# Optimization experiments

Hardware: AMD Instinct MI355X
Metric: run time of the kernel (lower is better)

## Reference

```python
import jax, jax.numpy as jnp
import numpy as np

B, S, D, H = 2, 4096, 512, 8
HD = D // H


def setup_inputs() -> dict:
    key = jax.random.key(0)
    ks = jax.random.split(key, 11)
    s = 1.0 / np.sqrt(D)
    return {
        "queries": jax.random.normal(ks[0], (B, S, D), jnp.float32),
        "keys": jax.random.normal(ks[1], (B, S, D), jnp.float32),
        "values": jax.random.normal(ks[2], (B, S, D), jnp.float32),
        "Wq": jax.random.normal(ks[3], (D, D), jnp.float32) * s,
        "bq": jnp.zeros((D,), jnp.float32),
        "Wk": jax.random.normal(ks[4], (D, D), jnp.float32) * s,
        "bk": jnp.zeros((D,), jnp.float32),
        "Wv": jax.random.normal(ks[5], (D, D), jnp.float32) * s,
        "bv": jnp.zeros((D,), jnp.float32),
        "Wo": jax.random.normal(ks[6], (D, D), jnp.float32) * s,
        "bo": jnp.zeros((D,), jnp.float32),
    }


def reference(queries, keys, values, Wq, bq, Wk, bk, Wv, bv, Wo, bo):
    b = queries.shape[0]
    # Linear projections (torch Linear: x @ W.T + b; here W stored as [in, out])
    q = (queries @ Wq + bq).reshape(b, -1, H, HD)   # [B, Sq, H, HD]
    k = (keys @ Wk + bk).reshape(b, -1, H, HD)       # [B, Sk, H, HD]
    v = (values @ Wv + bv).reshape(b, -1, H, HD)     # [B, Sk, H, HD]
    logits = jnp.einsum('bqhd,bkhd->bhqk', q, k) / jnp.sqrt(jnp.float32(HD))
    attn = jax.nn.softmax(logits, axis=-1)           # [B, H, Sq, Sk]  (dropout_rate=0 -> identity)
    ctx = jnp.einsum('bhqk,bkhd->bqhd', attn, v).reshape(b, -1, H * HD)
    return ctx @ Wo + bo
```

## Files before the change

### kernel.cpp

```cpp
#include <hip/hip_runtime.h>
#include <hip/hip_bf16.h>

constexpr int B_  = 2;
constexpr int S_  = 4096;
constexpr int D_  = 512;
constexpr int H_  = 8;
constexpr int HD_ = 64;
constexpr int M_  = B_ * S_;

typedef __attribute__((ext_vector_type(8))) short short8;
typedef __attribute__((ext_vector_type(4))) float floatx4;

static __device__ __forceinline__ unsigned short f2bf(float f) {
    union { float f; unsigned u; } v; v.f = f;
    unsigned r = v.u + 0x7fffu + ((v.u >> 16) & 1u);
    return (unsigned short)(r >> 16);
}

static __device__ __forceinline__ unsigned pk2bf(float a, float b) {
#if __has_builtin(__builtin_amdgcn_cvt_pk_bf16_f32)
    typedef __attribute__((ext_vector_type(2))) __bf16 bf16x2_t;
    union { bf16x2_t v; unsigned u; } u;
    u.v = __builtin_amdgcn_cvt_pk_bf16_f32(a, b);
    return u.u;
#else
    return (unsigned)f2bf(a) | ((unsigned)f2bf(b) << 16);
#endif
}

#if __has_builtin(__builtin_amdgcn_exp2f)
#define EXP2(x) __builtin_amdgcn_exp2f(x)
#else
#define EXP2(x) exp2f(x)
#endif

#define QSCALE 0.18033688011110204f

static __device__ __forceinline__ void gl_lds16(const void* g, void* l) {
    typedef __attribute__((address_space(1))) const unsigned GU;
    typedef __attribute__((address_space(3))) unsigned LU;
    __builtin_amdgcn_global_load_lds((GU*)g, (LU*)l, 16, 0, 0);
}

__global__ __launch_bounds__(256) void xcast_kernel(
    const float* __restrict__ Xq, const float* __restrict__ Xk, const float* __restrict__ Xv,
    unsigned short* __restrict__ Y) {
    const int z = blockIdx.z;
    const float* X = z == 0 ? Xq : (z == 1 ? Xk : Xv);
    unsigned short* Yz = Y + (size_t)z * M_ * D_;
    const int n8 = M_ * D_ / 8;
    int i = blockIdx.x * 256 + threadIdx.x;
    const int stride = gridDim.x * 256;
    for (; i < n8; i += stride) {
        float4 a = *(const float4*)&X[(size_t)i * 8];
        float4 b = *(const float4*)&X[(size_t)i * 8 + 4];
        union { short8 s; unsigned u[4]; } p;
        p.u[0] = pk2bf(a.x, a.y); p.u[1] = pk2bf(a.z, a.w);
        p.u[2] = pk2bf(b.x, b.y); p.u[3] = pk2bf(b.z, b.w);
        *(short8*)&Yz[(size_t)i * 8] = p.s;
    }
}

__global__ __launch_bounds__(256) void wtrans_kernel(
    const float* __restrict__ Wq, const float* __restrict__ Wk,
    const float* __restrict__ Wv, const float* __restrict__ Wo,
    unsigned short* __restrict__ Tq, unsigned short* __restrict__ Tk,
    unsigned short* __restrict__ Tv, unsigned short* __restrict__ To) {
    const int z = blockIdx.z;
    const float* W = z == 0 ? Wq : (z == 1 ? Wk : (z == 2 ? Wv : Wo));
    unsigned short* Wt = z == 0 ? Tq : (z == 1 ? Tk : (z == 2 ? Tv : To));
    __shared__ float T[64][65];
    const int t = threadIdx.x;
    const int k0 = blockIdx.x * 64, n0 = blockIdx.y * 64;
#pragma unroll
    for (int i = 0; i < 4; ++i) {
        const int flat = t + 256 * i;
        const int kr = flat >> 4, nc = (flat & 15) * 4;
        float4 v = *(const float4*)&W[(size_t)(k0 + kr) * 512 + n0 + nc];
        T[kr][nc] = v.x; T[kr][nc + 1] = v.y; T[kr][nc + 2] = v.z; T[kr][nc + 3] = v.w;
    }
    __syncthreads();
#pragma unroll
    for (int i = 0; i < 4; ++i) {
        const int flat = t + 256 * i;
        const int nr = flat >> 4, kc = (flat & 15) * 4;
        ushort4 o4;
        o4.x = f2bf(T[kc][nr]);     o4.y = f2bf(T[kc + 1][nr]);
        o4.z = f2bf(T[kc + 2][nr]); o4.w = f2bf(T[kc + 3][nr]);
        *(ushort4*)&Wt[(size_t)(n0 + nr) * 512 + k0 + kc] = o4;
    }
}

template <int MODE>
__global__ __launch_bounds__(256, 3) void gemm_kernel(
    const unsigned short* __restrict__ Ab,
    const unsigned short* __restrict__ Wt,
    const float* __restrict__ b0, const float* __restrict__ b1, const float* __restrict__ b2,
    unsigned short* __restrict__ o0, unsigned short* __restrict__ o1,
    unsigned short* __restrict__ o2, float* __restrict__ of) {
    __shared__ unsigned short As[128 * 64];
    __shared__ unsigned short Bs[128 * 64];

    const int tid  = threadIdx.x;
    const int w    = tid >> 6;
    const int lane = tid & 63;
    const int n0   = blockIdx.x * 128;
    const int m0   = blockIdx.y * 128;
    const int lm   = lane & 15;
    const int lq   = lane >> 4;
    const int wm   = (w >> 1) * 64;
    const int wn   = (w & 1) * 64;

    const int z = MODE == 0 ? (n0 >> 9) : 0;
    const unsigned short* A = MODE == 0 ? Ab + (size_t)z * M_ * D_ : Ab;

    const int srow = lane >> 3;
    const int sch  = lane & 7;
    const int ca   = (sch ^ (srow & 7)) * 8;

    floatx4 acc[4][4];
#pragma unroll
    for (int i = 0; i < 4; ++i)
#pragma unroll
        for (int j = 0; j < 4; ++j) acc[i][j] = (floatx4)0.0f;

    for (int kb = 0; kb < 8; ++kb) {
        const int k0 = kb * 64;
        __syncthreads();
#pragma unroll
        for (int it = 0; it < 4; ++it) {
            const int r8 = w * 32 + it * 8;
            gl_lds16(&A [(size_t)(m0 + r8 + srow) * 512 + k0 + ca], &As[r8 * 64]);
            gl_lds16(&Wt[(size_t)(n0 + r8 + srow) * 512 + k0 + ca], &Bs[r8 * 64]);
        }
        __syncthreads();

        short8 af[2][4], bf[2][4];
#pragma unroll
        for (int ks = 0; ks < 2; ++ks)
#pragma unroll
            for (int i = 0; i < 4; ++i) {
                const int cc = ((ks * 4 + lq) ^ (lm & 7)) * 8;
                af[ks][i] = *(const short8*)&As[(wm + i * 16 + lm) * 64 + cc];
                bf[ks][i] = *(const short8*)&Bs[(wn + i * 16 + lm) * 64 + cc];
            }
#pragma unroll
        for (int ks = 0; ks < 2; ++ks)
#pragma unroll
            for (int mi = 0; mi < 4; ++mi)
#pragma unroll
                for (int ni = 0; ni < 4; ++ni)
                    acc[mi][ni] = __builtin_amdgcn_mfma_f32_16x16x32_bf16(
                        af[ks][mi], bf[ks][ni], acc[mi][ni], 0, 0, 0);
    }

    const float* bias = MODE == 0 ? (z == 0 ? b0 : (z == 1 ? b1 : b2)) : b0;
    const float scale = (MODE == 0 && z == 0) ? QSCALE : 1.0f;
    const int nl0 = n0 & 511;

    float bias_n[4];
#pragma unroll
    for (int ni = 0; ni < 4; ++ni) bias_n[ni] = bias[nl0 + wn + ni * 16 + lm];

#pragma unroll
    for (int mi = 0; mi < 4; ++mi) {
#pragma unroll
        for (int ni = 0; ni < 4; ++ni) {
            if (MODE == 1) {
                const int gn = n0 + wn + ni * 16 + lm;
#pragma unroll
                for (int r = 0; r < 4; ++r) {
                    const int gm = m0 + wm + mi * 16 + lq * 4 + r;
                    of[(size_t)gm * 512 + gn] = acc[mi][ni][r] + bias_n[ni];
                }
            } else {
                const int gnl = nl0 + wn + ni * 16 + lm;
                const int h = gnl >> 6, hd = gnl & 63;
                if (z == 2) {
                    const int gm = m0 + wm + mi * 16 + lq * 4;
                    const int b = gm >> 12, s = gm & 4095;
                    union { ushort4 s4; uint2 u; } o4;
                    o4.u.x = pk2bf(acc[mi][ni][0] + bias_n[ni], acc[mi][ni][1] + bias_n[ni]);
                    o4.u.y = pk2bf(acc[mi][ni][2] + bias_n[ni], acc[mi][ni][3] + bias_n[ni]);
                    *(ushort4*)&o2[(((size_t)(b * 8 + h)) * 64 + hd) * 4096 + s] = o4.s4;
                } else {
                    unsigned short* out = z == 0 ? o0 : o1;
#pragma unroll
                    for (int r = 0; r < 4; ++r) {
                        const int gm = m0 + wm + mi * 16 + lq * 4 + r;
                        const int b = gm >> 12, s = gm & 4095;
                        const float vv = (acc[mi][ni][r] + bias_n[ni]) * scale;
                        out[(((size_t)(b * 8 + h)) * 4096 + s) * 64 + hd] = f2bf(vv);
                    }
                }
            }
        }
    }
}

__global__ __launch_bounds__(256, 2) void flash_kernel(
    const unsigned short* __restrict__ Q, const unsigned short* __restrict__ K,
    const unsigned short* __restrict__ Vt, unsigned short* __restrict__ ctx) {
    __shared__ unsigned short Ks[64 * 64];
    __shared__ unsigned short Vs[64 * 64];
    __shared__ unsigned short Ps[4][16 * 64];

    const int tid = threadIdx.x;
    const int w   = tid >> 6;
    const int l   = tid & 63;
    const int lm  = l & 15;
    const int lq  = l >> 4;
    const int q0  = blockIdx.x * 128;
    const int bh  = blockIdx.y;

    const size_t base = (size_t)bh * S_ * HD_;
    const unsigned short* Qg = Q + base;
    const unsigned short* Kg = K + base;
    const unsigned short* Vg = Vt + base;

    short8 qf[2][2];
#pragma unroll
    for (int qn = 0; qn < 2; ++qn) {
        const unsigned short* qp = &Qg[(size_t)(q0 + w * 32 + qn * 16 + lm) * 64];
        qf[qn][0] = *(const short8*)(qp + lq * 8);
        qf[qn][1] = *(const short8*)(qp + 32 + lq * 8);
    }

    short8 ones;
#pragma unroll
    for (int j = 0; j < 8; ++j) ones[j] = (short)0x3F80;

    floatx4 o[2][4];
#pragma unroll
    for (int qn = 0; qn < 2; ++qn)
#pragma unroll
        for (int i = 0; i < 4; ++i) o[qn][i] = (floatx4)0.0f;
    floatx4 ls[2];
    ls[0] = (floatx4)0.0f; ls[1] = (floatx4)0.0f;

    const int sr  = tid >> 3, sch = tid & 7;
    const int sw0 = sr * 64 + ((sch ^ (sr & 7)) * 8);
    const int sw1 = (sr + 32) * 64 + ((sch ^ (sr & 7)) * 8);
    const int lm7 = lm & 7;

    short8 kr0, kr1, vr0, vr1;
    kr0 = *(const short8*)&Kg[(size_t)sr * 64 + sch * 8];
    kr1 = *(const short8*)&Kg[(size_t)(sr + 32) * 64 + sch * 8];
    vr0 = *(const short8*)&Vg[(size_t)sr * S_ + sch * 8];
    vr1 = *(const short8*)&Vg[(size_t)(sr + 32) * S_ + sch * 8];

    for (int kt = 0; kt < 64; ++kt) {
        __syncthreads();
        *(short8*)&Ks[sw0] = kr0;
        *(short8*)&Ks[sw1] = kr1;
        *(short8*)&Vs[sw0] = vr0;
        *(short8*)&Vs[sw1] = vr1;
        __syncthreads();
        if (kt < 63) {
            const int t1 = (kt + 1) * 64;
            kr0 = *(const short8*)&Kg[(size_t)(t1 + sr) * 64 + sch * 8];
            kr1 = *(const short8*)&Kg[(size_t)(t1 + sr + 32) * 64 + sch * 8];
            vr0 = *(const short8*)&Vg[(size_t)sr * S_ + t1 + sch * 8];
            vr1 = *(const short8*)&Vg[(size_t)(sr + 32) * S_ + t1 + sch * 8];
        }

        short8 kf[2][4];
#pragma unroll
        for (int ks = 0; ks < 2; ++ks)
#pragma unroll
            for (int ni = 0; ni < 4; ++ni)
                kf[ks][ni] = *(const short8*)&Ks[(ni * 16 + lm) * 64 +
                                                 (((ks * 4 + lq) ^ lm7) * 8)];

        floatx4 sf[2][4];
#pragma unroll
        for (int qn = 0; qn < 2; ++qn)
#pragma unroll
            for (int ni = 0; ni < 4; ++ni) sf[qn][ni] = (floatx4)0.0f;
#pragma unroll
        for (int ks = 0; ks < 2; ++ks)
#pragma unroll
            for (int qn = 0; qn < 2; ++qn)
#pragma unroll
                for (int ni = 0; ni < 4; ++ni)
                    sf[qn][ni] = __builtin_amdgcn_mfma_f32_16x16x32_bf16(
                        kf[ks][ni], qf[qn][ks], sf[qn][ni], 0, 0, 0);

        short8 vf[2][4];
#pragma unroll
        for (int c = 0; c < 2; ++c)
#pragma unroll
            for (int ni = 0; ni < 4; ++ni)
                vf[c][ni] = *(const short8*)&Vs[(ni * 16 + lm) * 64 +
                                                (((c * 4 + lq) ^ lm7) * 8)];

        unsigned short* Pw = &Ps[w][0];
#pragma unroll
        for (int qn = 0; qn < 2; ++qn) {
#pragma unroll
            for (int ni = 0; ni < 4; ++ni) {
                uint2 pv;
                pv.x = pk2bf(EXP2(sf[qn][ni][0]), EXP2(sf[qn][ni][1]));
                pv.y = pk2bf(EXP2(sf[qn][ni][2]), EXP2(sf[qn][ni][3]));
                *(uint2*)&Pw[lm * 64 + (((ni * 2 + (lq >> 1)) ^ lm7) * 8) + (lq & 1) * 4] = pv;
            }
#pragma unroll
            for (int c = 0; c < 2; ++c) {
                short8 pf = *(const short8*)&Pw[lm * 64 + (((c * 4 + lq) ^ lm7) * 8)];
                ls[qn] = __builtin_amdgcn_mfma_f32_16x16x32_bf16(ones, pf, ls[qn], 0, 0, 0);
#pragma unroll
                for (int ni = 0; ni < 4; ++ni)
                    o[qn][ni] = __builtin_amdgcn_mfma_f32_16x16x32_bf16(
                        vf[c][ni], pf, o[qn][ni], 0, 0, 0);
            }
        }
    }

    const int b = bh >> 3, h = bh & 7;
#pragma unroll
    for (int qn = 0; qn < 2; ++qn) {
        const float inv = 1.0f / ls[qn][0];
        const int q = q0 + w * 32 + qn * 16 + lm;
        const size_t rb = ((size_t)(b * S_ + q)) * 512 + h * 64;
#pragma unroll
        for (int ni = 0; ni < 4; ++ni) {
            union { ushort4 s; uint2 u; } o4;
            o4.u.x = pk2bf(o[qn][ni][0] * inv, o[qn][ni][1] * inv);
            o4.u.y = pk2bf(o[qn][ni][2] * inv, o[qn][ni][3] * inv);
            *(ushort4*)&ctx[rb + ni * 16 + lq * 4] = o4.s;
        }
    }
}

extern "C" void kernel_launch(void* const* d_in, const int* in_sizes, int n_in,
                              void* d_out, int out_size, void* d_ws, size_t ws_size,
                              hipStream_t stream) {
    const float* queries = (const float*)d_in[0];
    const float* keys    = (const float*)d_in[1];
    const float* values  = (const float*)d_in[2];
    const float* Wq = (const float*)d_in[3];
    const float* bq = (const float*)d_in[4];
    const float* Wk = (const float*)d_in[5];
    const float* bk = (const float*)d_in[6];
    const float* Wv = (const float*)d_in[7];
    const float* bv = (const float*)d_in[8];
    const float* Wo = (const float*)d_in[9];
    const float* bo = (const float*)d_in[10];

    unsigned short* xb    = (unsigned short*)d_ws;
    unsigned short* wsctx = xb;
    unsigned short* wsq   = xb   + (size_t)3 * M_ * D_;
    unsigned short* wsk   = wsq  + (size_t)M_ * D_;
    unsigned short* wsvt  = wsk  + (size_t)M_ * D_;
    unsigned short* wtq   = wsvt + (size_t)M_ * D_;
    unsigned short* wtk   = wtq  + (size_t)D_ * D_;
    unsigned short* wtv   = wtk  + (size_t)D_ * D_;
    unsigned short* wto   = wtv  + (size_t)D_ * D_;

    xcast_kernel<<<dim3(1024, 1, 3), dim3(256), 0, stream>>>(queries, keys, values, xb);
    wtrans_kernel<<<dim3(8, 8, 4), dim3(256), 0, stream>>>(
        Wq, Wk, Wv, Wo, wtq, wtk, wtv, wto);

    gemm_kernel<0><<<dim3(12, 64), dim3(256), 0, stream>>>(
        xb, wtq, bq, bk, bv, wsq, wsk, wsvt, nullptr);

    flash_kernel<<<dim3(S_ / 128, B_ * H_), dim3(256), 0, stream>>>(wsq, wsk, wsvt, wsctx);

    gemm_kernel<1><<<dim3(4, 64), dim3(256), 0, stream>>>(
        wsctx, wto, bo, nullptr, nullptr, nullptr, nullptr, nullptr, (float*)d_out);
}
```

Before: 243.8 us.

## Double-buffer flash K/V via direct LDS loads and keep P in registers

The flash kernel now stages K and V tiles into double-buffered shared memory with global_load_lds, prefetching the next tile while computing the current one, which removes the register round trip and one barrier per iteration. The softmax probabilities stay in registers and feed 16x16x16 bf16 MFMAs directly instead of being written to and re-read from an LDS scratch tile. Q and K are now stored row-major [B,S,D] by the projection GEMM so the flash kernel reads them with strided row addressing. The trade-off is double the LDS footprint, a dropped occupancy hint, and smaller-K MFMAs that issue more instructions for the PV product.

```diff
diff --git a/kernel.cpp b/kernel.cpp
--- a/kernel.cpp
+++ b/kernel.cpp
@@ -9,6 +9,7 @@
 constexpr int M_  = B_ * S_;
 
 typedef __attribute__((ext_vector_type(8))) short short8;
+typedef __attribute__((ext_vector_type(4))) short short4v;
 typedef __attribute__((ext_vector_type(4))) float floatx4;
 
 static __device__ __forceinline__ unsigned short f2bf(float f) {
@@ -32,6 +33,18 @@
 #define EXP2(x) __builtin_amdgcn_exp2f(x)
 #else
 #define EXP2(x) exp2f(x)
+#endif
+
+#if __has_builtin(__builtin_amdgcn_mfma_f32_16x16x16bf16_1k)
+static __device__ __forceinline__ floatx4 mfma16k(short4v a, short4v b, floatx4 c) {
+    return __builtin_amdgcn_mfma_f32_16x16x16bf16_1k(a, b, c, 0, 0, 0);
+}
+#else
+static __device__ __forceinline__ floatx4 mfma16k(short4v a, short4v b, floatx4 c) {
+    short8 a8 = {a[0], a[1], a[2], a[3], 0, 0, 0, 0};
+    short8 b8 = {b[0], b[1], b[2], b[3], 0, 0, 0, 0};
+    return __builtin_amdgcn_mfma_f32_16x16x32_bf16(a8, b8, c, 0, 0, 0);
+}
 #endif
 
 #define QSCALE 0.18033688011110204f
@@ -108,6 +121,7 @@
     const int m0   = blockIdx.y * 128;
     const int lm   = lane & 15;
     const int lq   = lane >> 4;
+    const int lm7  = lm & 7;
     const int wm   = (w >> 1) * 64;
     const int wn   = (w & 1) * 64;
 
@@ -115,8 +129,7 @@
     const unsigned short* A = MODE == 0 ? Ab + (size_t)z * M_ * D_ : Ab;
 
     const int srow = lane >> 3;
-    const int sch  = lane & 7;
-    const int ca   = (sch ^ (srow & 7)) * 8;
+    const int slc  = ((lane & 7) ^ (srow & 7)) * 8;
 
     floatx4 acc[4][4];
 #pragma unroll
@@ -130,8 +143,8 @@
 #pragma unroll
         for (int it = 0; it < 4; ++it) {
             const int r8 = w * 32 + it * 8;
-            gl_lds16(&A [(size_t)(m0 + r8 + srow) * 512 + k0 + ca], &As[r8 * 64]);
-            gl_lds16(&Wt[(size_t)(n0 + r8 + srow) * 512 + k0 + ca], &Bs[r8 * 64]);
+            gl_lds16(&A [(size_t)(m0 + r8 + srow) * 512 + k0 + slc], &As[r8 * 64]);
+            gl_lds16(&Wt[(size_t)(n0 + r8 + srow) * 512 + k0 + slc], &Bs[r8 * 64]);
         }
         __syncthreads();
 
@@ -140,7 +153,7 @@
         for (int ks = 0; ks < 2; ++ks)
 #pragma unroll
             for (int i = 0; i < 4; ++i) {
-                const int cc = ((ks * 4 + lq) ^ (lm & 7)) * 8;
+                const int cc = ((ks * 4 + lq) ^ lm7) * 8;
                 af[ks][i] = *(const short8*)&As[(wm + i * 16 + lm) * 64 + cc];
                 bf[ks][i] = *(const short8*)&Bs[(wn + i * 16 + lm) * 64 + cc];
             }
@@ -175,8 +188,8 @@
                 }
             } else {
                 const int gnl = nl0 + wn + ni * 16 + lm;
-                const int h = gnl >> 6, hd = gnl & 63;
                 if (z == 2) {
+                    const int h = gnl >> 6, hd = gnl & 63;
                     const int gm = m0 + wm + mi * 16 + lq * 4;
                     const int b = gm >> 12, s = gm & 4095;
                     union { ushort4 s4; uint2 u; } o4;
@@ -188,9 +201,8 @@
 #pragma unroll
                     for (int r = 0; r < 4; ++r) {
                         const int gm = m0 + wm + mi * 16 + lq * 4 + r;
-                        const int b = gm >> 12, s = gm & 4095;
-                        const float vv = (acc[mi][ni][r] + bias_n[ni]) * scale;
-                        out[(((size_t)(b * 8 + h)) * 4096 + s) * 64 + hd] = f2bf(vv);
+                        out[(size_t)gm * 512 + gnl] =
+                            f2bf((acc[mi][ni][r] + bias_n[ni]) * scale);
                     }
                 }
             }
@@ -198,37 +210,37 @@
     }
 }
 
-__global__ __launch_bounds__(256, 2) void flash_kernel(
+__global__ __launch_bounds__(256) void flash_kernel(
     const unsigned short* __restrict__ Q, const unsigned short* __restrict__ K,
     const unsigned short* __restrict__ Vt, unsigned short* __restrict__ ctx) {
-    __shared__ unsigned short Ks[64 * 64];
-    __shared__ unsigned short Vs[64 * 64];
-    __shared__ unsigned short Ps[4][16 * 64];
+    __shared__ unsigned short Ks[2][64 * 64];
+    __shared__ unsigned short Vs[2][64 * 64];
 
     const int tid = threadIdx.x;
     const int w   = tid >> 6;
     const int l   = tid & 63;
     const int lm  = l & 15;
     const int lq  = l >> 4;
+    const int lm7 = lm & 7;
     const int q0  = blockIdx.x * 128;
     const int bh  = blockIdx.y;
-
-    const size_t base = (size_t)bh * S_ * HD_;
-    const unsigned short* Qg = Q + base;
-    const unsigned short* Kg = K + base;
-    const unsigned short* Vg = Vt + base;
+    const int b   = bh >> 3, h = bh & 7;
+
+    const unsigned short* Vg = Vt + (size_t)bh * HD_ * S_;
+    const size_t rowbase = (size_t)b * 4096;
 
     short8 qf[2][2];
 #pragma unroll
     for (int qn = 0; qn < 2; ++qn) {
-        const unsigned short* qp = &Qg[(size_t)(q0 + w * 32 + qn * 16 + lm) * 64];
+        const unsigned short* qp =
+            &Q[(rowbase + q0 + w * 32 + qn * 16 + lm) * 512 + h * 64];
         qf[qn][0] = *(const short8*)(qp + lq * 8);
         qf[qn][1] = *(const short8*)(qp + 32 + lq * 8);
     }
 
-    short8 ones;
-#pragma unroll
-    for (int j = 0; j < 8; ++j) ones[j] = (short)0x3F80;
+    short4v ones4;
+#pragma unroll
+    for (int j = 0; j < 4; ++j) ones4[j] = (short)0x3F80;
 
     floatx4 o[2][4];
 #pragma unroll
@@ -238,96 +250,85 @@
     floatx4 ls[2];
     ls[0] = (floatx4)0.0f; ls[1] = (floatx4)0.0f;
 
-    const int sr  = tid >> 3, sch = tid & 7;
-    const int sw0 = sr * 64 + ((sch ^ (sr & 7)) * 8);
-    const int sw1 = (sr + 32) * 64 + ((sch ^ (sr & 7)) * 8);
-    const int lm7 = lm & 7;
-
-    short8 kr0, kr1, vr0, vr1;
-    kr0 = *(const short8*)&Kg[(size_t)sr * 64 + sch * 8];
-    kr1 = *(const short8*)&Kg[(size_t)(sr + 32) * 64 + sch * 8];
-    vr0 = *(const short8*)&Vg[(size_t)sr * S_ + sch * 8];
-    vr1 = *(const short8*)&Vg[(size_t)(sr + 32) * S_ + sch * 8];
+    const int srow = l >> 3;
+    const int slc  = ((l & 7) ^ (srow & 7)) * 8;
+
+#define STAGE(T0, BUF)                                                         \
+    {                                                                          \
+        _Pragma("unroll") for (int it = 0; it < 2; ++it) {                     \
+            const int r8 = w * 16 + it * 8;                                    \
+            gl_lds16(&K[(rowbase + (T0) + r8 + srow) * 512 + h * 64 + slc],    \
+                     &Ks[BUF][r8 * 64]);                                       \
+            gl_lds16(&Vg[(size_t)(r8 + srow) * 4096 + (T0) + slc],            \
+                     &Vs[BUF][r8 * 64]);                                       \
+        }                                                                      \
+    }
+
+    STAGE(0, 0);
+    __syncthreads();
 
     for (int kt = 0; kt < 64; ++kt) {
-        __syncthreads();
-        *(short8*)&Ks[sw0] = kr0;
-        *(short8*)&Ks[sw1] = kr1;
-        *(short8*)&Vs[sw0] = vr0;
-        *(short8*)&Vs[sw1] = vr1;
-        __syncthreads();
-        if (kt < 63) {
-            const int t1 = (kt + 1) * 64;
-            kr0 = *(const short8*)&Kg[(size_t)(t1 + sr) * 64 + sch * 8];
-            kr1 = *(const short8*)&Kg[(size_t)(t1 + sr + 32) * 64 + sch * 8];
-            vr0 = *(const short8*)&Vg[(size_t)sr * S_ + t1 + sch * 8];
-            vr1 = *(const short8*)&Vg[(size_t)(sr + 32) * S_ + t1 + sch * 8];
-        }
+        const int cur = kt & 1;
+        if (kt < 63) STAGE((kt + 1) * 64, cur ^ 1);
 
         short8 kf[2][4];
 #pragma unroll
         for (int ks = 0; ks < 2; ++ks)
 #pragma unroll
             for (int ni = 0; ni < 4; ++ni)
-                kf[ks][ni] = *(const short8*)&Ks[(ni * 16 + lm) * 64 +
-                                                 (((ks * 4 + lq) ^ lm7) * 8)];
-
-        floatx4 sf[2][4];
-#pragma unroll
-        for (int qn = 0; qn < 2; ++qn)
-#pragma unroll
-            for (int ni = 0; ni < 4; ++ni) sf[qn][ni] = (floatx4)0.0f;
-#pragma unroll
-        for (int ks = 0; ks < 2; ++ks)
-#pragma unroll
-            for (int qn = 0; qn < 2; ++qn)
+                kf[ks][ni] = *(const short8*)&Ks[cur][(ni * 16 + lm) * 64 +
+                                                      (((ks * 4 + lq) ^ lm7) * 8)];
+        short4v vfr[4][4];
+#pragma unroll
+        for (int mt = 0; mt < 4; ++mt)
+#pragma unroll
+            for (int ni = 0; ni < 4; ++ni)
+                vfr[mt][ni] = *(const short4v*)&Vs[cur][(mt * 16 + lm) * 64 +
+                                                        (((ni * 2 + (lq >> 1)) ^ lm7) * 8) +
+                                                        (lq & 1) * 4];
+
+#pragma unroll
+        for (int qn = 0; qn < 2; ++qn) {
+            floatx4 sf[4];
+#pragma unroll
+            for (int ni = 0; ni < 4; ++ni) sf[ni] = (floatx4)0.0f;
+#pragma unroll
+            for (int ks = 0; ks < 2; ++ks)
 #pragma unroll
                 for (int ni = 0; ni < 4; ++ni)
-                    sf[qn][ni] = __builtin_amdgcn_mfma_f32_16x16x32_bf16(
-                        kf[ks][ni], qf[qn][ks], sf[qn][ni], 0, 0, 0);
-
-        short8 vf[2][4];
-#pragma unroll
-        for (int c = 0; c < 2; ++c)
-#pragma unroll
-            for (int ni = 0; ni < 4; ++ni)
-                vf[c][ni] = *(const short8*)&Vs[(ni * 16 + lm) * 64 +
-                                                (((c * 4 + lq) ^ lm7) * 8)];
-
-        unsigned short* Pw = &Ps[w][0];
-#pragma unroll
-        for (int qn = 0; qn < 2; ++qn) {
+                    sf[ni] = __builtin_amdgcn_mfma_f32_16x16x32_bf16(
+                        kf[ks][ni], qf[qn][ks], sf[ni], 0, 0, 0);
+
+            short4v pp[4];
 #pragma unroll
             for (int ni = 0; ni < 4; ++ni) {
-                uint2 pv;
-                pv.x = pk2bf(EXP2(sf[qn][ni][0]), EXP2(sf[qn][ni][1]));
-                pv.y = pk2bf(EXP2(sf[qn][ni][2]), EXP2(sf[qn][ni][3]));
-                *(uint2*)&Pw[lm * 64 + (((ni * 2 + (lq >> 1)) ^ lm7) * 8) + (lq & 1) * 4] = pv;
+                union { short4v s; unsigned u[2]; } t;
+                t.u[0] = pk2bf(EXP2(sf[ni][0]), EXP2(sf[ni][1]));
+                t.u[1] = pk2bf(EXP2(sf[ni][2]), EXP2(sf[ni][3]));
+                pp[ni] = t.s;
             }
 #pragma unroll
-            for (int c = 0; c < 2; ++c) {
-                short8 pf = *(const short8*)&Pw[lm * 64 + (((c * 4 + lq) ^ lm7) * 8)];
-                ls[qn] = __builtin_amdgcn_mfma_f32_16x16x32_bf16(ones, pf, ls[qn], 0, 0, 0);
-#pragma unroll
-                for (int ni = 0; ni < 4; ++ni)
-                    o[qn][ni] = __builtin_amdgcn_mfma_f32_16x16x32_bf16(
-                        vf[c][ni], pf, o[qn][ni], 0, 0, 0);
+            for (int ni = 0; ni < 4; ++ni) {
+                ls[qn] = mfma16k(ones4, pp[ni], ls[qn]);
+#pragma unroll
+                for (int mt = 0; mt < 4; ++mt)
+                    o[qn][mt] = mfma16k(vfr[mt][ni], pp[ni], o[qn][mt]);
             }
         }
-    }
-
-    const int b = bh >> 3, h = bh & 7;
+        __syncthreads();
+    }
+
 #pragma unroll
     for (int qn = 0; qn < 2; ++qn) {
         const float inv = 1.0f / ls[qn][0];
         const int q = q0 + w * 32 + qn * 16 + lm;
-        const size_t rb = ((size_t)(b * S_ + q)) * 512 + h * 64;
-#pragma unroll
-        for (int ni = 0; ni < 4; ++ni) {
+        const size_t rb = (rowbase + q) * 512 + h * 64;
+#pragma unroll
+        for (int mt = 0; mt < 4; ++mt) {
             union { ushort4 s; uint2 u; } o4;
-            o4.u.x = pk2bf(o[qn][ni][0] * inv, o[qn][ni][1] * inv);
-            o4.u.y = pk2bf(o[qn][ni][2] * inv, o[qn][ni][3] * inv);
-            *(ushort4*)&ctx[rb + ni * 16 + lq * 4] = o4.s;
+            o4.u.x = pk2bf(o[qn][mt][0] * inv, o[qn][mt][1] * inv);
+            o4.u.y = pk2bf(o[qn][mt][2] * inv, o[qn][mt][3] * inv);
+            *(ushort4*)&ctx[rb + mt * 16 + lq * 4] = o4.s;
         }
     }
 }
@@ -364,7 +365,8 @@
     gemm_kernel<0><<<dim3(12, 64), dim3(256), 0, stream>>>(
         xb, wtq, bq, bk, bv, wsq, wsk, wsvt, nullptr);
 
-    flash_kernel<<<dim3(S_ / 128, B_ * H_), dim3(256), 0, stream>>>(wsq, wsk, wsvt, wsctx);
+    flash_kernel<<<dim3(S_ / 128, B_ * H_), dim3(256), 0, stream>>>(
+        wsq, wsk, wsvt, wsctx);
 
     gemm_kernel<1><<<dim3(4, 64), dim3(256), 0, stream>>>(
         wsctx, wto, bo, nullptr, nullptr, nullptr, nullptr, nullptr, (float*)d_out);
```

Result: slower. 265.2 us (+8.8%).
